# Kernel optimization log

Measured on AMD Instinct MI355X. Metric: run time of the kernel, lower is better.

The kernel has to match this reference:

```python
import jax, jax.numpy as jnp
import numpy as np
from jax import lax

RF, NLF, MESH, FUSION = 64, 16, 16, 64


def _conv3x3(x, w, b):
    # stride 1, pad 1, ksize 3 == SAME
    y = lax.conv_general_dilated(x, w, (1, 1), 'SAME',
                                 dimension_numbers=('NCHW', 'OIHW', 'NCHW'))
    return y + b[None, :, None, None]


def _bn(x, g, b, m, v, eps=1e-5):
    scale = g / jnp.sqrt(v + eps)
    return (x - m[None, :, None, None]) * scale[None, :, None, None] + b[None, :, None, None]


def _rct_block(x, w1, b1, g, be, m, v, w2, b2):
    # extra_conv=True: Conv -> BN -> SiLU -> Conv (all stride 1)
    h = jax.nn.silu(_bn(_conv3x3(x, w1, b1), g, be, m, v))
    return _conv3x3(h, w2, b2)


def setup_inputs():
    key = jax.random.key(0)
    ks = jax.random.split(key, 8)
    B, H, W = 4, 512, 512
    return {
        'feature': jax.random.normal(ks[0], (B, RF, H, W), jnp.float32),
        'p_low': jax.random.normal(ks[1], (B, FUSION, MESH + 1, MESH + 1), jnp.float32),
        'r_w1': jax.random.normal(ks[2], (FUSION, FUSION, 3, 3), jnp.float32) * 0.05,
        'r_b1': jnp.zeros((FUSION,), jnp.float32),
        'r_gamma': jnp.ones((FUSION,), jnp.float32),
        'r_beta': jnp.zeros((FUSION,), jnp.float32),
        'r_mean': jnp.zeros((FUSION,), jnp.float32),
        'r_var': jnp.ones((FUSION,), jnp.float32),
        'r_w2': jax.random.normal(ks[3], (RF * NLF, FUSION, 3, 3), jnp.float32) * 0.05,
        'r_b2': jnp.zeros((RF * NLF,), jnp.float32),
        't_w1': jax.random.normal(ks[4], (FUSION, FUSION, 3, 3), jnp.float32) * 0.05,
        't_b1': jnp.zeros((FUSION,), jnp.float32),
        't_gamma': jnp.ones((FUSION,), jnp.float32),
        't_beta': jnp.zeros((FUSION,), jnp.float32),
        't_mean': jnp.zeros((FUSION,), jnp.float32),
        't_var': jnp.ones((FUSION,), jnp.float32),
        't_w2': jax.random.normal(ks[5], (3 * NLF, FUSION, 3, 3), jnp.float32) * 0.05,
        't_b2': jnp.zeros((3 * NLF,), jnp.float32),
    }


def reference(feature, p_low, r_w1, r_b1, r_gamma, r_beta, r_mean, r_var, r_w2, r_b2,
              t_w1, t_b1, t_gamma, t_beta, t_mean, t_var, t_w2, t_b2):
    B, C, H, W = feature.shape
    M = MESH
    mh, mw = H // M, W // M  # H,W divisible by mesh_size -> pad_tensor is identity
    P = mh * mw

    r_l = _rct_block(p_low, r_w1, r_b1, r_gamma, r_beta, r_mean, r_var, r_w2, r_b2)  # [B, RF*NLF, M+1, M+1]
    t_l = _rct_block(p_low, t_w1, t_b1, t_gamma, t_beta, t_mean, t_var, t_w2, t_b2)  # [B, 3*NLF, M+1, M+1]

    # channel dim factors as (feat, nlf); corners concat along nlf axis in order
    # (i,j), (i,j+1), (i+1,j), (i+1,j+1) -> K = 4*NLF keys per tile
    rc = r_l.reshape(B, RF, NLF, M + 1, M + 1)
    rk = jnp.concatenate([rc[..., :M, :M], rc[..., :M, 1:],
                          rc[..., 1:, :M], rc[..., 1:, 1:]], axis=2)  # [B,RF,4NLF,M,M]
    tc = t_l.reshape(B, 3, NLF, M + 1, M + 1)
    tk = jnp.concatenate([tc[..., :M, :M], tc[..., :M, 1:],
                          tc[..., 1:, :M], tc[..., 1:, 1:]], axis=2)  # [B,3,4NLF,M,M]

    # split feature into tiles: [B, M, M, P, RF] (row-major pixel order within tile)
    f = feature.reshape(B, RF, M, mh, M, mw).transpose(0, 2, 4, 3, 5, 1).reshape(B, M, M, P, RF)

    scale = 1.0 / jnp.sqrt(jnp.float32(RF))
    att = jnp.einsum('bxypr,brkxy->bxypk', f, rk) * scale  # [B,M,M,P,4NLF]
    att = jax.nn.softmax(att, axis=-1)
    out = jnp.einsum('bxypk,bckxy->bxycp', att, tk)  # [B,M,M,3,P]

    Y = out.reshape(B, M, M, 3, mh, mw).transpose(0, 3, 1, 4, 2, 5).reshape(B, 3, H, W)
    return Y
```

## Files before the change

kernel.cpp:

```cpp
#include <hip/hip_runtime.h>

typedef unsigned short u16;
typedef __bf16 bf16x8 __attribute__((ext_vector_type(8)));
typedef unsigned short us8 __attribute__((ext_vector_type(8)));
typedef float f32x4 __attribute__((ext_vector_type(4)));
typedef float f32x2 __attribute__((ext_vector_type(2)));
typedef unsigned int u32x4 __attribute__((ext_vector_type(4)));

union U8u { us8 s; u16 u[8]; };

__device__ __forceinline__ u16 f2bf(float f){
  unsigned u = __builtin_bit_cast(unsigned, f);
  u += 0x7fffu + ((u >> 16) & 1u);
  return (u16)(u >> 16);
}
__device__ __forceinline__ bf16x8 asbf(us8 x){ return __builtin_bit_cast(bf16x8, x); }

#define MFMA16(a,b,c) __builtin_amdgcn_mfma_f32_16x16x32_bf16((a),(b),(c),0,0,0)

__device__ __forceinline__ void stage_zero2(u16* sS, int tid){
  uint* z = (uint*)sS;
  for (int i = tid; i < 12996; i += 256) z[i] = 0u;
}

__device__ __forceinline__ void stage_src_f32T(const float* __restrict__ src,
                                               u16* sS, int tid){
  for (int i4 = tid; i4 < 4624; i4 += 256){
    int e = i4 * 4;
    f32x4 dv = *(const f32x4*)(src + e);
    #pragma unroll
    for (int t = 0; t < 4; t++){
      int ee = e + t;
      int ci = ee / 289; int rr = ee - ci*289;
      int oy = rr / 17;  int ox = rr - oy*17;
      sS[((oy+1)*19 + ox+1)*72 + ci] = f2bf(dv[t]);
    }
  }
}

__device__ __forceinline__ void stage_src_pm(const u16* __restrict__ src,
                                             u16* sS, int tid){
  for (int i8 = tid; i8 < 2312; i8 += 256){
    int pix = i8 >> 3, c0 = (i8 & 7) << 3;
    us8 v = *(const us8*)(src + ((size_t)pix << 6) + c0);
    int oy = pix / 17, ox = pix - oy*17;
    *(us8*)(sS + ((oy+1)*19 + ox+1)*72 + c0) = v;
  }
}

__device__ __forceinline__ void stage_w_f32(const float* __restrict__ w, int m0,
                                            u16* sW, int tid){
  for (int i4 = tid; i4 < 2304; i4 += 256){
    int e = i4 * 4;
    int co = e / 576; int r0 = e - co*576;
    f32x4 wv = *(const f32x4*)(w + (size_t)(m0+co)*576 + r0);
    #pragma unroll
    for (int t = 0; t < 4; t++){
      int r = r0 + t; int cin = r / 9; int tap = r - cin*9;
      sW[co*584 + tap*64 + cin] = f2bf(wv[t]);
    }
  }
}

__device__ __forceinline__ f32x4 conv_tile2(const u16* sS, const u16* sW,
                                            int nt, int l15, int q)
{
  int p = nt*16 + l15; int pc = p > 288 ? 288 : p;
  int oy = pc / 17, ox = pc - oy*17;
  f32x4 acc = {0.f, 0.f, 0.f, 0.f};
  #pragma unroll
  for (int ks = 0; ks < 18; ks++){
    const int tap = ks >> 1;
    const int dy = tap / 3, dx = tap - dy*3;
    int pix2 = (oy+dy)*19 + (ox+dx);
    us8 bv = *(const us8*)(sS + pix2*72 + (ks & 1)*32 + q*8);
    us8 av = *(const us8*)(sW + l15*584 + ks*32 + q*8);
    acc = MFMA16(asbf(av), asbf(bv), acc);
  }
  return acc;
}

__global__ __launch_bounds__(256) void conv1_k(
    const float* __restrict__ p_low,
    const float* __restrict__ wR, const float* __restrict__ b1R,
    const float* __restrict__ gR, const float* __restrict__ beR,
    const float* __restrict__ mR, const float* __restrict__ vR,
    const float* __restrict__ wT, const float* __restrict__ b1T,
    const float* __restrict__ gT, const float* __restrict__ beT,
    const float* __restrict__ mT, const float* __restrict__ vT,
    u16* __restrict__ hR, u16* __restrict__ hT)
{
  __shared__ __attribute__((aligned(16))) u16 sS[25992];
  __shared__ __attribute__((aligned(16))) u16 sW[9344];
  int tid = threadIdx.x;
  int bx = blockIdx.x;
  int job = bx >> 6;
  int b = (bx >> 4) & 3;
  int m0 = ((bx >> 2) & 3) << 4;
  int px = bx & 3;
  int nt0 = px * 5, ntEnd = nt0 + 5 > 19 ? 19 : nt0 + 5;
  const float* w  = job ? wT  : wR;
  const float* b1 = job ? b1T : b1R;
  const float* g  = job ? gT  : gR;
  const float* be = job ? beT : beR;
  const float* mn = job ? mT  : mR;
  const float* vr = job ? vT  : vR;
  u16* out = job ? hT : hR;
  const float* src = p_low + (size_t)b * 18496;

  stage_zero2(sS, tid);
  __syncthreads();
  stage_src_f32T(src, sS, tid);
  stage_w_f32(w, m0, sW, tid);
  __syncthreads();

  int lane = tid & 63, wave = tid >> 6;
  int l15 = lane & 15, q = lane >> 4;
  float scl[4], sft[4];
  #pragma unroll
  for (int e = 0; e < 4; e++){
    int co = m0 + q*4 + e;
    float s = g[co] / sqrtf(vr[co] + 1e-5f);
    scl[e] = s;
    sft[e] = (b1[co] - mn[co]) * s + be[co];
  }
  for (int nt = nt0 + wave; nt < ntEnd; nt += 4){
    f32x4 acc = conv_tile2(sS, sW, nt, l15, q);
    int p = nt*16 + l15;
    if (p < 289){
      float si[4];
      #pragma unroll
      for (int e = 0; e < 4; e++){
        float y = acc[e]*scl[e] + sft[e];
        si[e] = y / (1.f + __expf(-y));
      }
      uint2 pk;
      pk.x = (uint)f2bf(si[0]) | ((uint)f2bf(si[1]) << 16);
      pk.y = (uint)f2bf(si[2]) | ((uint)f2bf(si[3]) << 16);
      *(uint2*)(out + ((size_t)b*289 + p)*64 + m0 + q*4) = pk;
    }
  }
}

__global__ __launch_bounds__(256) void conv2_k(
    const u16* __restrict__ hR, const u16* __restrict__ hT,
    const float* __restrict__ w2R, const float* __restrict__ b2R,
    const float* __restrict__ w2T, const float* __restrict__ b2T,
    u16* __restrict__ rlq, float* __restrict__ tlq)
{
  __shared__ __attribute__((aligned(16))) u16 sS[25992];
  __shared__ __attribute__((aligned(16))) u16 sW[9344];
  int tid = threadIdx.x;
  int bx = blockIdx.x;
  const float *w, *bias; const u16* src;
  int b, m0, isR;
  if (bx < 256){
    isR = 1; b = bx >> 6; m0 = (bx & 63) << 4;
    src = hR + (size_t)b*18496; w = w2R; bias = b2R;
  } else {
    isR = 0; int i = bx - 256; b = i / 3; m0 = (i - b*3) << 4;
    src = hT + (size_t)b*18496; w = w2T; bias = b2T;
  }

  stage_zero2(sS, tid);
  __syncthreads();
  stage_src_pm(src, sS, tid);
  stage_w_f32(w, m0, sW, tid);
  __syncthreads();

  int lane = tid & 63, wave = tid >> 6;
  int l15 = lane & 15, q = lane >> 4;
  float bs[4];
  #pragma unroll
  for (int e = 0; e < 4; e++) bs[e] = bias[m0 + q*4 + e];
  const float PSC = 0.18033688f;
  for (int nt = wave; nt < 19; nt += 4){
    f32x4 acc = conv_tile2(sS, sW, nt, l15, q);
    int p = nt*16 + l15;
    if (p < 289){
      if (isR){
        uint2 pk;
        pk.x = (uint)f2bf((acc[0]+bs[0])*PSC)
             | ((uint)f2bf((acc[1]+bs[1])*PSC) << 16);
        pk.y = (uint)f2bf((acc[2]+bs[2])*PSC)
             | ((uint)f2bf((acc[3]+bs[3])*PSC) << 16);
        *(uint2*)(rlq + ((size_t)b*289 + p)*1024 + m0 + q*4) = pk;
      } else {
        f32x4 ov = {acc[0]+bs[0], acc[1]+bs[1], acc[2]+bs[2], acc[3]+bs[3]};
        *(f32x4*)(tlq + ((size_t)b*289 + p)*48 + m0 + q*4) = ov;
      }
    }
  }
}

__global__ __launch_bounds__(256) void attn_k(
    const uint* __restrict__ feat,
    const u16* __restrict__ rlq, const float* __restrict__ tlq,
    float* __restrict__ out)
{
  __shared__ __attribute__((aligned(16))) u16 rkT[4608];
  __shared__ __attribute__((aligned(16))) float tkF[256];
  __shared__ __attribute__((aligned(1024))) uint sF[8192];
  int tid = threadIdx.x;
  int ty = blockIdx.x, tx = blockIdx.y, b = blockIdx.z;
  int lane = tid & 63, wave = tid >> 6;
  int l15 = lane & 15, q = lane >> 4;

  {
    int corner = wave;
    int pix = (tx + (corner >> 1))*17 + ty + (corner & 1);
    const u16* sp = rlq + ((size_t)b*289 + pix)*1024 + lane*16;
    U8u v0, v1; v0.s = *(const us8*)sp; v1.s = *(const us8*)(sp + 8);
    #pragma unroll
    for (int nl = 0; nl < 8; nl++){
      rkT[(corner*16 + nl)*72 + lane]     = v0.u[nl];
      rkT[(corner*16 + 8 + nl)*72 + lane] = v1.u[nl];
    }
  }
  if (tid < 192){
    int corner = tid / 48; int idx = tid - corner*48;
    int pix = (tx + (corner >> 1))*17 + ty + (corner & 1);
    int c = idx >> 4, nl = idx & 15;
    tkF[c*64 + corner*16 + nl] = tlq[((size_t)b*289 + pix)*48 + idx];
  }
  __syncthreads();

  bf16x8 frk[4][2];
  #pragma unroll
  for (int nt = 0; nt < 4; nt++)
    #pragma unroll
    for (int ks = 0; ks < 2; ks++)
      frk[nt][ks] = __builtin_bit_cast(bf16x8,
          *(const us8*)(rkT + (nt*16 + l15)*72 + ks*32 + q*8));

  const float* __restrict__ tkq = tkF + q*4;

  const size_t HW = (size_t)512*512;
  int segl = (wave << 3) + (lane >> 3);
  int part = lane & 7;

  for (int c = 0; c < 8; ++c){
    #pragma unroll
    for (int p = 0; p < 8; ++p){
      int seg = p*32 + segl;
      int i  = seg >> 6;
      int ch = seg & 63;
      int qq = (ch >> 3) & 3;
      int col0 = ((part ^ (qq << 1)) << 2);
      const uint* src = feat + ((size_t)(b*64 + ch))*HW
                      + (size_t)(tx*32 + i*8 + c)*512 + (ty*32 + col0);
      uint* dst = sF + (size_t)(p*32 + (wave << 3))*32;
      __builtin_amdgcn_global_load_lds(
          (const __attribute__((address_space(1))) void*)src,
          (__attribute__((address_space(3))) void*)dst, 16, 0, 0);
    }
    __syncthreads();

    #pragma unroll
    for (int h = 0; h < 2; ++h){
      int colL = ((h << 4) + l15) ^ (q << 3);
      const uint* fp = sF + wave*2048 + q*256 + colL;
      uint r0[8], r1[8];
      #pragma unroll
      for (int j = 0; j < 8; j++){
        r0[j] = fp[j*32];
        r1[j] = fp[1024 + j*32];
      }
      u32x4 p0v, p1v;
      #pragma unroll
      for (int j2 = 0; j2 < 4; j2++){
        p0v[j2] = __builtin_amdgcn_perm(r0[2*j2+1], r0[2*j2], 0x07060302u);
        p1v[j2] = __builtin_amdgcn_perm(r1[2*j2+1], r1[2*j2], 0x07060302u);
      }
      bf16x8 A0 = __builtin_bit_cast(bf16x8, p0v);
      bf16x8 A1 = __builtin_bit_cast(bf16x8, p1v);

      f32x4 acc[4];
      #pragma unroll
      for (int nt = 0; nt < 4; nt++){
        f32x4 zz = {0.f, 0.f, 0.f, 0.f};
        zz = MFMA16(frk[nt][0], A0, zz);
        zz = MFMA16(frk[nt][1], A1, zz);
        acc[nt] = zz;
      }

      f32x2 den2 = {0.f,0.f}, o0v = {0.f,0.f}, o1v = {0.f,0.f}, o2v = {0.f,0.f};
      #pragma unroll
      for (int nt = 0; nt < 4; nt++){
        f32x4 t0 = *(const f32x4*)(tkq + 0*64 + nt*16);
        f32x4 t1 = *(const f32x4*)(tkq + 1*64 + nt*16);
        f32x4 t2 = *(const f32x4*)(tkq + 2*64 + nt*16);
        f32x2 pa, pb;
        pa[0] = __builtin_amdgcn_exp2f(acc[nt][0]);
        pa[1] = __builtin_amdgcn_exp2f(acc[nt][1]);
        pb[0] = __builtin_amdgcn_exp2f(acc[nt][2]);
        pb[1] = __builtin_amdgcn_exp2f(acc[nt][3]);
        den2 += pa; den2 += pb;
        f32x2 t0a = {t0[0], t0[1]}, t0b = {t0[2], t0[3]};
        f32x2 t1a = {t1[0], t1[1]}, t1b = {t1[2], t1[3]};
        f32x2 t2a = {t2[0], t2[1]}, t2b = {t2[2], t2[3]};
        o0v = __builtin_elementwise_fma(pa, t0a, o0v);
        o0v = __builtin_elementwise_fma(pb, t0b, o0v);
        o1v = __builtin_elementwise_fma(pa, t1a, o1v);
        o1v = __builtin_elementwise_fma(pb, t1b, o1v);
        o2v = __builtin_elementwise_fma(pa, t2a, o2v);
        o2v = __builtin_elementwise_fma(pb, t2b, o2v);
      }
      float den = den2[0] + den2[1];
      float o0 = o0v[0] + o0v[1];
      float o1 = o1v[0] + o1v[1];
      float o2 = o2v[0] + o2v[1];
      o0  += __shfl_xor(o0, 16, 64);
      o1  += __shfl_xor(o1, 16, 64);
      o2  += __shfl_xor(o2, 16, 64);
      den += __shfl_xor(den, 16, 64);
      o0  += __shfl_xor(o0, 32, 64);
      o1  += __shfl_xor(o1, 32, 64);
      o2  += __shfl_xor(o2, 32, 64);
      den += __shfl_xor(den, 32, 64);
      float rin = __builtin_amdgcn_rcpf(den);
      float val = (q == 0) ? o0 : ((q == 1) ? o1 : o2);
      int hh = tx*32 + wave*8 + c;
      int j0 = h << 4;
      if (q < 3)
        out[((size_t)(b*3 + q)*512 + hh)*512 + (ty*32 + j0 + l15)] = val * rin;
    }
    __syncthreads();
  }
}

extern "C" void kernel_launch(void* const* d_in, const int* in_sizes, int n_in,
                              void* d_out, int out_size, void* d_ws, size_t ws_size,
                              hipStream_t stream)
{
  (void)in_sizes; (void)n_in; (void)out_size; (void)ws_size;
  const uint*  feature = (const uint*)d_in[0];
  const float* p_low = (const float*)d_in[1];
  const float* r_w1 = (const float*)d_in[2];
  const float* r_b1 = (const float*)d_in[3];
  const float* r_g  = (const float*)d_in[4];
  const float* r_be = (const float*)d_in[5];
  const float* r_m  = (const float*)d_in[6];
  const float* r_v  = (const float*)d_in[7];
  const float* r_w2 = (const float*)d_in[8];
  const float* r_b2 = (const float*)d_in[9];
  const float* t_w1 = (const float*)d_in[10];
  const float* t_b1 = (const float*)d_in[11];
  const float* t_g  = (const float*)d_in[12];
  const float* t_be = (const float*)d_in[13];
  const float* t_m  = (const float*)d_in[14];
  const float* t_v  = (const float*)d_in[15];
  const float* t_w2 = (const float*)d_in[16];
  const float* t_b2 = (const float*)d_in[17];

  char* ws = (char*)d_ws;
  u16* hR = (u16*)ws;
  u16* hT = hR + (size_t)4*289*64;
  u16* rlq = (u16*)(ws + 295936);
  float* tlq = (float*)(ws + 295936 + 2367488);
  float* outp = (float*)d_out;

  hipLaunchKernelGGL(conv1_k, dim3(128), dim3(256), 0, stream,
      p_low, r_w1, r_b1, r_g, r_be, r_m, r_v,
      t_w1, t_b1, t_g, t_be, t_m, t_v, hR, hT);
  hipLaunchKernelGGL(conv2_k, dim3(268), dim3(256), 0, stream,
      hR, hT, r_w2, r_b2, t_w2, t_b2, rlq, tlq);
  hipLaunchKernelGGL(attn_k, dim3(16, 16, 4), dim3(256), 0, stream,
      feature, rlq, tlq, outp);
}
```

Baseline: 442.0 us.

## Double-buffer feature tiles in attention kernel and hoist tk values into registers

The attention kernel now uses two LDS buffers for feature rows. The next row's global-to-LDS loads are issued right after the current buffer has been read into registers, so the loads overlap with the MFMA, exp and output work instead of sitting behind a barrier. The tk corner values are also loaded once into registers rather than re-read from LDS on every iteration. This doubles LDS use for sF to 64KB and raises register pressure, which may lower occupancy.

```diff
diff --git a/kernel.cpp b/kernel.cpp
--- a/kernel.cpp
+++ b/kernel.cpp
@@ -200,7 +200,7 @@
 {
   __shared__ __attribute__((aligned(16))) u16 rkT[4608];
   __shared__ __attribute__((aligned(16))) float tkF[256];
-  __shared__ __attribute__((aligned(1024))) uint sF[8192];
+  __shared__ __attribute__((aligned(1024))) uint sF[2][8192];
   int tid = threadIdx.x;
   int ty = blockIdx.x, tx = blockIdx.y, b = blockIdx.z;
   int lane = tid & 63, wave = tid >> 6;
@@ -233,44 +233,59 @@
       frk[nt][ks] = __builtin_bit_cast(bf16x8,
           *(const us8*)(rkT + (nt*16 + l15)*72 + ks*32 + q*8));
 
-  const float* __restrict__ tkq = tkF + q*4;
+  f32x4 tkc[3][4];
+  #pragma unroll
+  for (int c = 0; c < 3; c++)
+    #pragma unroll
+    for (int nt = 0; nt < 4; nt++)
+      tkc[c][nt] = *(const f32x4*)(tkF + c*64 + nt*16 + q*4);
 
   const size_t HW = (size_t)512*512;
   int segl = (wave << 3) + (lane >> 3);
   int part = lane & 7;
 
+  #define STAGE(c_, bb_)                                                     \
+    _Pragma("unroll")                                                        \
+    for (int p = 0; p < 8; ++p){                                             \
+      int seg = p*32 + segl;                                                 \
+      int i  = seg >> 6;                                                     \
+      int ch = seg & 63;                                                     \
+      int qq = (ch >> 3) & 3;                                                \
+      int col0 = ((part ^ (qq << 1)) << 2);                                  \
+      const uint* src = feat + ((size_t)(b*64 + ch))*HW                      \
+                      + (size_t)(tx*32 + i*8 + (c_))*512 + (ty*32 + col0);   \
+      uint* dst = sF[bb_] + (size_t)(p*32 + (wave << 3))*32;                 \
+      __builtin_amdgcn_global_load_lds(                                      \
+          (const __attribute__((address_space(1))) void*)src,                \
+          (__attribute__((address_space(3))) void*)dst, 16, 0, 0);           \
+    }
+
+  STAGE(0, 0);
+  __syncthreads();
+
   for (int c = 0; c < 8; ++c){
-    #pragma unroll
-    for (int p = 0; p < 8; ++p){
-      int seg = p*32 + segl;
-      int i  = seg >> 6;
-      int ch = seg & 63;
-      int qq = (ch >> 3) & 3;
-      int col0 = ((part ^ (qq << 1)) << 2);
-      const uint* src = feat + ((size_t)(b*64 + ch))*HW
-                      + (size_t)(tx*32 + i*8 + c)*512 + (ty*32 + col0);
-      uint* dst = sF + (size_t)(p*32 + (wave << 3))*32;
-      __builtin_amdgcn_global_load_lds(
-          (const __attribute__((address_space(1))) void*)src,
-          (__attribute__((address_space(3))) void*)dst, 16, 0, 0);
-    }
-    __syncthreads();
-
+    int bb = c & 1;
+    uint r0[2][8], r1[2][8];
     #pragma unroll
     for (int h = 0; h < 2; ++h){
       int colL = ((h << 4) + l15) ^ (q << 3);
-      const uint* fp = sF + wave*2048 + q*256 + colL;
-      uint r0[8], r1[8];
+      const uint* fp = sF[bb] + wave*2048 + q*256 + colL;
       #pragma unroll
       for (int j = 0; j < 8; j++){
-        r0[j] = fp[j*32];
-        r1[j] = fp[1024 + j*32];
-      }
+        r0[h][j] = fp[j*32];
+        r1[h][j] = fp[1024 + j*32];
+      }
+    }
+    if (c < 7){ STAGE(c+1, bb^1); }
+    __builtin_amdgcn_sched_barrier(0);
+
+    #pragma unroll
+    for (int h = 0; h < 2; ++h){
       u32x4 p0v, p1v;
       #pragma unroll
       for (int j2 = 0; j2 < 4; j2++){
-        p0v[j2] = __builtin_amdgcn_perm(r0[2*j2+1], r0[2*j2], 0x07060302u);
-        p1v[j2] = __builtin_amdgcn_perm(r1[2*j2+1], r1[2*j2], 0x07060302u);
+        p0v[j2] = __builtin_amdgcn_perm(r0[h][2*j2+1], r0[h][2*j2], 0x07060302u);
+        p1v[j2] = __builtin_amdgcn_perm(r1[h][2*j2+1], r1[h][2*j2], 0x07060302u);
       }
       bf16x8 A0 = __builtin_bit_cast(bf16x8, p0v);
       bf16x8 A1 = __builtin_bit_cast(bf16x8, p1v);
@@ -287,18 +302,18 @@
       f32x2 den2 = {0.f,0.f}, o0v = {0.f,0.f}, o1v = {0.f,0.f}, o2v = {0.f,0.f};
       #pragma unroll
       for (int nt = 0; nt < 4; nt++){
-        f32x4 t0 = *(const f32x4*)(tkq + 0*64 + nt*16);
-        f32x4 t1 = *(const f32x4*)(tkq + 1*64 + nt*16);
-        f32x4 t2 = *(const f32x4*)(tkq + 2*64 + nt*16);
         f32x2 pa, pb;
         pa[0] = __builtin_amdgcn_exp2f(acc[nt][0]);
         pa[1] = __builtin_amdgcn_exp2f(acc[nt][1]);
         pb[0] = __builtin_amdgcn_exp2f(acc[nt][2]);
         pb[1] = __builtin_amdgcn_exp2f(acc[nt][3]);
         den2 += pa; den2 += pb;
-        f32x2 t0a = {t0[0], t0[1]}, t0b = {t0[2], t0[3]};
-        f32x2 t1a = {t1[0], t1[1]}, t1b = {t1[2], t1[3]};
-        f32x2 t2a = {t2[0], t2[1]}, t2b = {t2[2], t2[3]};
+        f32x2 t0a = {tkc[0][nt][0], tkc[0][nt][1]};
+        f32x2 t0b = {tkc[0][nt][2], tkc[0][nt][3]};
+        f32x2 t1a = {tkc[1][nt][0], tkc[1][nt][1]};
+        f32x2 t1b = {tkc[1][nt][2], tkc[1][nt][3]};
+        f32x2 t2a = {tkc[2][nt][0], tkc[2][nt][1]};
+        f32x2 t2b = {tkc[2][nt][2], tkc[2][nt][3]};
         o0v = __builtin_elementwise_fma(pa, t0a, o0v);
         o0v = __builtin_elementwise_fma(pb, t0b, o0v);
         o1v = __builtin_elementwise_fma(pa, t1a, o1v);
@@ -327,6 +342,7 @@
     }
     __syncthreads();
   }
+  #undef STAGE
 }
 
 extern "C" void kernel_launch(void* const* d_in, const int* in_sizes, int n_in,
```

After: 435.3 us (median of 2 runs). About the same (-1.5%).
